# Performance work log

Hardware: AMD Instinct MI355X
Metric: run time of the kernel (lower is better)

## Reference

```python
import jax, jax.numpy as jnp
import numpy as np

VOX = 0.1
XMIN, YMIN, ZMIN = -20.0, -20.0, -2.0
XMAX, YMAX, ZMAX = 20.0, 20.0, 3.0
GX, GY = 400, 400          # grid size from (40m / 0.1m)
P = 32                     # max_points_per_voxel
K = 60000                  # max_num_voxels
N = 2_000_000              # total points
B = 4                      # batch size
SUB = 120                  # points drawn from a 120x120 sub-grid so uniques (<=57600) <= K


def setup_inputs() -> dict:
    key = jax.random.key(0)
    kb, kx, ky, kz, ki, ku, kv = jax.random.split(key, 7)
    b = jax.random.randint(kb, (N,), 0, B).astype(jnp.float32)
    xi = jax.random.randint(kx, (N,), 0, SUB).astype(jnp.float32)
    yi = jax.random.randint(ky, (N,), 0, SUB).astype(jnp.float32)
    ux = jax.random.uniform(ku, (N,))
    uy = jax.random.uniform(kv, (N,))
    x = XMIN + (xi + ux * 0.999) * VOX
    y = YMIN + (yi + uy * 0.999) * VOX
    z = jax.random.uniform(kz, (N,), minval=ZMIN, maxval=ZMAX - 1e-3)
    r = jax.random.uniform(ki, (N,))
    points = jnp.stack([b, x, y, z, r], axis=1)  # [N,5]
    return {"points": points, "batch_size": B}


def reference(points, batch_size):
    # in-range mask (identity for our generated data, but kept for fidelity)
    mask = ((points[:, 1] >= XMIN) & (points[:, 1] < XMAX)
            & (points[:, 2] >= YMIN) & (points[:, 2] < YMAX)
            & (points[:, 3] >= ZMIN) & (points[:, 3] < ZMAX))
    bi = points[:, 0].astype(jnp.int32)
    xi = jnp.clip(((points[:, 1] - XMIN) / VOX).astype(jnp.int32), 0, GX - 1)
    yi = jnp.clip(((points[:, 2] - YMIN) / VOX).astype(jnp.int32), 0, GY - 1)
    # flat voxel id; numeric order == lexicographic (b,x,y) order as in torch.unique(dim=0)
    flat = bi * (GX * GY) + xi * GY + yi
    sentinel = jnp.int32(batch_size * GX * GY)
    flat = jnp.where(mask, flat, sentinel)
    uniq, inv = jnp.unique(flat, size=K, fill_value=sentinel, return_inverse=True)
    inv = inv.astype(jnp.int32)

    # points per voxel (clamped to slot capacity)
    counts = jax.ops.segment_sum(mask.astype(jnp.int32), inv, num_segments=K)
    counts = jnp.minimum(counts, P)

    # slot = rank of each point within its voxel, in original point order
    order = jnp.argsort(inv)                      # stable
    sinv = inv[order]
    first = jnp.searchsorted(sinv, sinv, side='left')
    ranks = (jnp.arange(N) - first).astype(jnp.int32)
    slot = jnp.zeros(N, jnp.int32).at[order].set(ranks)

    # scatter point features into fixed-size voxel slots; overflow/out-of-range dropped
    rows = jnp.where(mask, inv, K)                # K is OOB -> dropped
    voxels = jnp.zeros((K, P, 4), points.dtype).at[rows, slot].set(
        points[:, 1:5], mode='drop')

    # decode sorted unique flat ids back to (batch, x, y)
    cb = uniq // (GX * GY)
    rem = uniq % (GX * GY)
    coors = jnp.stack([cb, rem // GY, rem % GY], axis=1)
    return voxels, counts, coors
```

## Files before the change

### kernel.cpp

```cpp
#include <hip/hip_runtime.h>

namespace {

constexpr int GX = 400, GY = 400;
constexpr int P = 32;
constexpr int K = 60000;
constexpr int MCAP = 128;
constexpr int NB = 4;
constexpr int NVOX = NB * GX * GY;
constexpr int SCAN_CHUNK = 1024;
constexpr int NBLK = (NVOX + 1 + SCAN_CHUNK - 1) / SCAN_CHUNK;
constexpr int OCC_PAD = NBLK * SCAN_CHUNK;

constexpr unsigned A20 = 0x779B1u;
constexpr unsigned mulinv20(unsigned a) {
  unsigned x = a;
  for (int i = 0; i < 6; ++i) x *= 2u - a * x;
  return x & 0xFFFFFu;
}
constexpr unsigned AINV20 = mulinv20(A20);
static_assert(((A20 * AINV20) & 0xFFFFFu) == 1u, "bad inverse");

constexpr int NBUK3 = 512;
constexpr int JH = 2048;
constexpr int CAP3 = 5120;
constexpr int PPB = 4096;
constexpr int IPT = PPB / 256;

constexpr float XMINf = -20.f, YMINf = -20.f, ZMINf = -2.f;
constexpr float XMAXf =  20.f, YMAXf =  20.f, ZMAXf =  3.f;

constexpr int OUT_CNT = K * P * 4;
constexpr int OUT_COR = OUT_CNT + K;

typedef float floatx2 __attribute__((ext_vector_type(2)));

__device__ __forceinline__ int bin_of(float v) {
  return (int)((v + 20.0f) * 10.0f);
}

__device__ __forceinline__ bool point_voxel(const float* __restrict__ pt, int& flat) {
  float x = pt[1], y = pt[2], z = pt[3];
  bool m = (x >= XMINf) & (x < XMAXf) & (y >= YMINf) & (y < YMAXf)
         & (z >= ZMINf) & (z < ZMAXf);
  if (!m) return false;
  int bi = (int)pt[0];
  int xi = min(max(bin_of(x), 0), GX - 1);
  int yi = min(max(bin_of(y), 0), GY - 1);
  flat = bi * (GX * GY) + xi * GY + yi;
  return true;
}

__device__ __forceinline__ unsigned bf16rne(float f) {
  unsigned u = __float_as_uint(f);
  return ((u + 0x7fffu + ((u >> 16) & 1u)) >> 16) & 0xffffu;
}
__device__ __forceinline__ float bf16dq(unsigned h) {
  return __uint_as_float(h << 16);
}

__global__ void __launch_bounds__(256) k_mark_bucket(
    const float* __restrict__ pts, int n, int* __restrict__ occ,
    int* __restrict__ bcur, unsigned* __restrict__ akey,
    uint2* __restrict__ afeat) {
  __shared__ int hist[512], lb[512], gb[512], ofs[512];
  __shared__ unsigned st[PPB];
  __shared__ uint2 stf[PPB];
  __shared__ unsigned short stb[PPB];
  __shared__ int ps[256];
  __shared__ int tot_s;
  int t = threadIdx.x;
  for (int j = t; j < 512; j += 256) hist[j] = 0;
  __syncthreads();

  int base = blockIdx.x * PPB;
  int bk[IPT]; unsigned rec[IPT]; uint2 ft[IPT];
  #pragma unroll
  for (int j = 0; j < IPT; ++j) {
    int i = base + j * 256 + t;
    bk[j] = -1;
    if (i < n) {
      const float* pp = pts + (size_t)i * 5;
      int flat;
      if (point_voxel(pp, flat)) {
        occ[flat] = 1;
        unsigned u = ((unsigned)flat * A20) & 0xFFFFFu;
        bk[j] = (int)(u >> 11);
        rec[j] = ((u & 0x7FFu) << 21) | (unsigned)i;
        ft[j].x = bf16rne(pp[1]) | (bf16rne(pp[2]) << 16);
        ft[j].y = bf16rne(pp[3]) | (bf16rne(pp[4]) << 16);
      }
    }
    if (bk[j] >= 0) atomicAdd(&hist[bk[j]], 1);
  }
  __syncthreads();
  int h0 = hist[2 * t], h1 = hist[2 * t + 1];
  int local = h0 + h1;
  ps[t] = local;
  __syncthreads();
  for (int o = 1; o < 256; o <<= 1) {
    int add = (t >= o) ? ps[t - o] : 0;
    __syncthreads();
    ps[t] += add;
    __syncthreads();
  }
  int excl = ps[t] - local;
  lb[2 * t] = excl;          ofs[2 * t] = excl;
  lb[2 * t + 1] = excl + h0; ofs[2 * t + 1] = excl + h0;
  if (t == 255) tot_s = ps[255];
  __syncthreads();
  #pragma unroll
  for (int j = 0; j < IPT; ++j) {
    if (bk[j] >= 0) {
      int pos = atomicAdd(&ofs[bk[j]], 1);
      st[pos] = rec[j];
      stf[pos] = ft[j];
      stb[pos] = (unsigned short)bk[j];
    }
  }
  __syncthreads();
  for (int b = t; b < NBUK3; b += 256) {
    int nb = hist[b];
    gb[b] = nb ? atomicAdd(&bcur[b], nb) : 0;
  }
  __syncthreads();
  int tot = tot_s;
  for (int e = t; e < tot; e += 256) {
    int b = stb[e];
    int dst = gb[b] + (e - lb[b]);
    if (dst < CAP3) {
      size_t a = (size_t)b * CAP3 + dst;
      akey[a] = st[e];
      afeat[a] = stf[e];
    }
  }
}

__global__ void k_bsum(const int* __restrict__ occ, int* __restrict__ bsum) {
  __shared__ int wsums[4];
  int t = threadIdx.x, wid = t >> 6, lane = t & 63;
  int base = blockIdx.x * SCAN_CHUNK;
  int4 v = ((const int4*)(occ + base))[t];
  int s = v.x + v.y + v.z + v.w;
  for (int o = 32; o > 0; o >>= 1) s += __shfl_xor(s, o, 64);
  if (lane == 0) wsums[wid] = s;
  __syncthreads();
  if (t == 0) bsum[blockIdx.x] = wsums[0] + wsums[1] + wsums[2] + wsums[3];
}

__global__ void k_scanb(int* __restrict__ bsum) {
  __shared__ int lds[1024];
  int t = threadIdx.x;
  int v = (t < NBLK) ? bsum[t] : 0;
  lds[t] = v;
  __syncthreads();
  for (int o = 1; o < 1024; o <<= 1) {
    int add = (t >= o) ? lds[t - o] : 0;
    __syncthreads();
    lds[t] += add;
    __syncthreads();
  }
  if (t < NBLK) bsum[t] = lds[t] - v;
  if (t == NBLK - 1) bsum[NBLK] = lds[t];
}

__global__ void k_rank(int* __restrict__ occ, const int* __restrict__ bsum,
                       int* __restrict__ uniq) {
  __shared__ int wsums[4];
  int t = threadIdx.x, wid = t >> 6, lane = t & 63;
  int base = blockIdx.x * SCAN_CHUNK;
  int4 v = ((const int4*)(occ + base))[t];
  int tsum = v.x + v.y + v.z + v.w;
  int sc = tsum;
  for (int o = 1; o < 64; o <<= 1) {
    int u = __shfl_up(sc, o, 64);
    if (lane >= o) sc += u;
  }
  if (lane == 63) wsums[wid] = sc;
  __syncthreads();
  int woff = 0;
  for (int w = 0; w < wid; ++w) woff += wsums[w];
  int p = bsum[blockIdx.x] + woff + (sc - tsum);
  int e0 = base + t * 4;
  int4 r;
  r.x = p; if (v.x) { if (p < K) uniq[p] = e0 + 0; ++p; }
  r.y = p; if (v.y) { if (p < K) uniq[p] = e0 + 1; ++p; }
  r.z = p; if (v.z) { if (p < K) uniq[p] = e0 + 2; ++p; }
  r.w = p; if (v.w) { if (p < K) uniq[p] = e0 + 3; ++p; }
  ((int4*)(occ + base))[t] = r;
}

__global__ void __launch_bounds__(256) k_build2(
    unsigned* __restrict__ akey, unsigned short* __restrict__ gpos,
    const int* __restrict__ bcur, const int* __restrict__ rank,
    const int* __restrict__ nuq_p, int* __restrict__ voxoff,
    int* __restrict__ vcnt) {
  __shared__ unsigned st[CAP3];
  __shared__ int hist[JH], scn[JH], cur[JH];
  __shared__ int ps[256];
  int b = blockIdx.x, t = threadIdx.x;
  int tot = min(bcur[b], CAP3);
  for (int j = t; j < JH; j += 256) hist[j] = 0;
  __syncthreads();
  unsigned* keys = akey + (size_t)b * CAP3;
  for (int i = t; i < tot; i += 256) {
    unsigned kk = keys[i];
    st[i] = kk;
    atomicAdd(&hist[kk >> 21], 1);
  }
  __syncthreads();
  int h[8]; int local = 0;
  #pragma unroll
  for (int u = 0; u < 8; ++u) { h[u] = hist[8 * t + u]; local += h[u]; }
  ps[t] = local;
  __syncthreads();
  for (int o = 1; o < 256; o <<= 1) {
    int add = (t >= o) ? ps[t - o] : 0;
    __syncthreads();
    ps[t] += add;
    __syncthreads();
  }
  int run = ps[t] - local;
  #pragma unroll
  for (int u = 0; u < 8; ++u) { scn[8 * t + u] = run; cur[8 * t + u] = run; run += h[u]; }
  __syncthreads();
  int cbase = b * CAP3;
  for (int i = t; i < tot; i += 256) {
    unsigned kk = st[i];
    int slot = atomicAdd(&cur[kk >> 21], 1);
    keys[slot] = kk & 0x1FFFFFu;
    gpos[cbase + slot] = (unsigned short)i;
  }
  int nq = min(nuq_p[0], K);
  for (int j = t; j < JH; j += 256) {
    if (hist[j] > 0) {
      unsigned u = ((unsigned)b << 11) | (unsigned)j;
      int flat = (int)((u * AINV20) & 0xFFFFFu);
      int k = rank[flat];
      if (k >= 0 && k < nq) {
        voxoff[k] = cbase + scn[j];
        vcnt[k] = hist[j];
      }
    }
  }
}

__global__ void __launch_bounds__(256) k_final_g(
    const unsigned* __restrict__ akey, const unsigned short* __restrict__ gpos,
    const uint2* __restrict__ afeat, const int* __restrict__ uniq,
    const int* __restrict__ voxoff, const int* __restrict__ vcnt,
    const int* __restrict__ nuq_p, float* __restrict__ out) {
  int wid = threadIdx.x >> 6, lane = threadIdx.x & 63;
  int k = blockIdx.x * 4 + wid;
  if (k >= K) return;
  int nq = min(nuq_p[0], K);
  const unsigned UMAX = 0xffffffffu;
  int s = lane >> 1, hh = lane & 1;

  int c_tot = 0, c_out = 0, off = 0;
  if (k < nq) {
    off = voxoff[k];
    int c = vcnt[k];
    c_tot = min(c, MCAP);
    c_out = min(c, P);
  }

  unsigned pos_s = 0u;
  if (c_tot > 0) {
    if (c_tot <= 64) {
      unsigned key = (lane < c_tot) ? akey[off + lane] : UMAX;
      unsigned pos = (lane < c_tot) ? (unsigned)gpos[off + lane] : 0u;
      for (int kk = 2; kk <= 64; kk <<= 1) {
        for (int d = kk >> 1; d >= 1; d >>= 1) {
          unsigned pk = __shfl_xor(key, d, 64);
          unsigned pq = __shfl_xor(pos, d, 64);
          bool tmin = ((lane & d) == 0) == ((lane & kk) == 0);
          bool sw = tmin ? (pk < key) : (pk > key);
          if (sw) { key = pk; pos = pq; }
        }
      }
      pos_s = __shfl(pos, s, 64);
    } else {
      unsigned k0 = (lane < c_tot) ? akey[off + lane] : UMAX;
      unsigned p0 = (lane < c_tot) ? (unsigned)gpos[off + lane] : 0u;
      unsigned k1 = (lane + 64 < c_tot) ? akey[off + 64 + lane] : UMAX;
      unsigned p1 = (lane + 64 < c_tot) ? (unsigned)gpos[off + 64 + lane] : 0u;
      #pragma unroll
      for (int ph = 1; ph <= 7; ++ph) {
        int kk = 1 << ph;
        bool up = ((lane & (kk >> 1)) == 0);
        #pragma unroll
        for (int d = kk >> 1; d >= 2; d >>= 1) {
          int dl = d >> 1;
          unsigned q0 = __shfl_xor(k0, dl, 64), r0 = __shfl_xor(p0, dl, 64);
          unsigned q1 = __shfl_xor(k1, dl, 64), r1 = __shfl_xor(p1, dl, 64);
          bool low = ((lane & dl) == 0);
          if (low == up) {
            if (q0 < k0) { k0 = q0; p0 = r0; }
            if (q1 < k1) { k1 = q1; p1 = r1; }
          } else {
            if (q0 > k0) { k0 = q0; p0 = r0; }
            if (q1 > k1) { k1 = q1; p1 = r1; }
          }
        }
        bool sw = up ? (k1 < k0) : (k1 > k0);
        if (sw) {
          unsigned tk = k0; k0 = k1; k1 = tk;
          unsigned tp = p0; p0 = p1; p1 = tp;
        }
      }
      unsigned a0 = __shfl(p0, s >> 1, 64);
      unsigned a1 = __shfl(p1, s >> 1, 64);
      pos_s = (s & 1) ? a1 : a0;
    }
  }

  uint2 fv = make_uint2(0u, 0u);
  if (s < c_out) {
    int b = off / CAP3;
    fv = afeat[(size_t)b * CAP3 + pos_s];
  }
  float va, vb;
  if (hh == 0) { va = bf16dq(fv.x & 0xffffu); vb = bf16dq(fv.x >> 16); }
  else         { va = bf16dq(fv.y & 0xffffu); vb = bf16dq(fv.y >> 16); }
  floatx2 val = {va, vb};
  __builtin_nontemporal_store(val, (floatx2*)(out + (size_t)k * (P * 4)) + lane);

  if (lane == 0) {
    out[OUT_CNT + k] = (float)c_out;
    int f = (k < nq) ? uniq[k] : NVOX;
    int cb = f / (GX * GY), rem = f % (GX * GY);
    out[OUT_COR + (size_t)k * 3 + 0] = (float)cb;
    out[OUT_COR + (size_t)k * 3 + 1] = (float)(rem / GY);
    out[OUT_COR + (size_t)k * 3 + 2] = (float)(rem % GY);
  }
}

__global__ void k_mark(const float* __restrict__ pts, int n,
                       int* __restrict__ occ, int* __restrict__ pflat) {
  int i = blockIdx.x * blockDim.x + threadIdx.x;
  if (i >= n) return;
  int flat = -1;
  if (point_voxel(pts + (size_t)i * 5, flat)) occ[flat] = 1;
  if (pflat) pflat[i] = flat;
}

__global__ void k_append(const int* __restrict__ pflat, int n,
                         const int* __restrict__ rank, int* __restrict__ cnt,
                         unsigned* __restrict__ vox) {
  int i = blockIdx.x * blockDim.x + threadIdx.x;
  if (i >= n) return;
  int f = pflat[i];
  if (f < 0) return;
  int v = rank[f];
  if (v >= K) return;
  int pos = atomicAdd(&cnt[v], 1);
  if (pos < MCAP) vox[(size_t)v * MCAP + pos] = (unsigned)i;
}

__global__ void k_append_fb(const float* __restrict__ pts, int n,
                            const int* __restrict__ rank, int* __restrict__ cnt,
                            unsigned* __restrict__ vox) {
  int i = blockIdx.x * blockDim.x + threadIdx.x;
  if (i >= n) return;
  int flat;
  if (!point_voxel(pts + (size_t)i * 5, flat)) return;
  int v = rank[flat];
  if (v >= K) return;
  int pos = atomicAdd(&cnt[v], 1);
  if (pos < MCAP) vox[(size_t)v * MCAP + pos] = (unsigned)i;
}

__global__ void __launch_bounds__(256) k_final_d(
    const float* __restrict__ pts, const int* __restrict__ uniq,
    const int* __restrict__ cnt, const int* __restrict__ nuq_p,
    float* __restrict__ out) {
  int wid = threadIdx.x >> 6, lane = threadIdx.x & 63;
  int k = blockIdx.x * 4 + wid;
  if (k >= K) return;
  int nuq = min(nuq_p[0], K);
  int c_tot = 0, c_out = 0;
  if (k < nuq) {
    int c = cnt[k];
    c_tot = min(c, MCAP);
    c_out = min(c, P);
  }
  const unsigned UMAX = 0xffffffffu;
  const unsigned* row = (const unsigned*)out + (size_t)k * MCAP;
  uint2 q = ((const uint2*)row)[lane];
  unsigned v0 = (2 * lane     < c_tot) ? q.x : UMAX;
  unsigned v1 = (2 * lane + 1 < c_tot) ? q.y : UMAX;
  #pragma unroll
  for (int ph = 1; ph <= 7; ++ph) {
    int kk = 1 << ph;
    bool up = ((lane & (kk >> 1)) == 0);
    #pragma unroll
    for (int d = kk >> 1; d >= 2; d >>= 1) {
      int dl = d >> 1;
      unsigned p0 = __shfl_xor(v0, dl, 64);
      unsigned p1 = __shfl_xor(v1, dl, 64);
      bool low = ((lane & dl) == 0);
      if (low == up) { v0 = min(v0, p0); v1 = min(v1, p1); }
      else           { v0 = max(v0, p0); v1 = max(v1, p1); }
    }
    unsigned lo = min(v0, v1), hi = max(v0, v1);
    v0 = up ? lo : hi;
    v1 = up ? hi : lo;
  }
  int mys = lane >> 1, h = lane & 1;
  unsigned a0 = __shfl(v0, mys >> 1, 64);
  unsigned a1 = __shfl(v1, mys >> 1, 64);
  unsigned myidx = (mys & 1) ? a1 : a0;
  float a = 0.f, b = 0.f;
  if (mys < c_out) {
    const float* pp = pts + (size_t)myidx * 5;
    a = pp[1 + 2 * h];
    b = pp[2 + 2 * h];
  }
  float2* vout = (float2*)(out + (size_t)k * (P * 4));
  vout[lane] = make_float2(a, b);
  if (lane == 0) {
    out[OUT_CNT + k] = (float)c_out;
    int f = (k < nuq) ? uniq[k] : NVOX;
    int cb = f / (GX * GY), rem = f % (GX * GY);
    out[OUT_COR + (size_t)k * 3 + 0] = (float)cb;
    out[OUT_COR + (size_t)k * 3 + 1] = (float)(rem / GY);
    out[OUT_COR + (size_t)k * 3 + 2] = (float)(rem % GY);
  }
}

}

extern "C" void kernel_launch(void* const* d_in, const int* in_sizes, int n_in,
                              void* d_out, int out_size, void* d_ws, size_t ws_size,
                              hipStream_t stream) {
  const float* pts = (const float*)d_in[0];
  int n = in_sizes[0] / 5;
  float* out = (float*)d_out;
  int nb_pts = (n + 255) / 256;

  size_t o_occ   = 0;
  size_t o_bsum  = o_occ + OCC_PAD;
  size_t o_uniq  = o_bsum + NBLK + 1;
  size_t o_voff  = o_uniq + K;
  size_t o_vcnt  = o_voff + K;
  size_t o_bcur  = o_vcnt + K;
  size_t o_akey  = (o_bcur + NBUK3 + 3) & ~(size_t)3;
  size_t o_afeat = o_akey + (size_t)NBUK3 * CAP3;
  size_t o_gpos  = o_afeat + (size_t)NBUK3 * CAP3 * 2;
  size_t totA    = o_gpos + ((size_t)NBUK3 * CAP3 + 1) / 2;

  if (ws_size >= totA * sizeof(int) && n <= (1 << 21)) {
    int* occ   = (int*)d_ws + o_occ;
    int* bsum  = (int*)d_ws + o_bsum;
    int* uniq  = (int*)d_ws + o_uniq;
    int* voff  = (int*)d_ws + o_voff;
    int* vcnt  = (int*)d_ws + o_vcnt;
    int* bcur  = (int*)d_ws + o_bcur;
    unsigned* akey = (unsigned*)((int*)d_ws + o_akey);
    uint2* afeat   = (uint2*)((int*)d_ws + o_afeat);
    unsigned short* gpos = (unsigned short*)((int*)d_ws + o_gpos);
    const int* nuq_p = bsum + NBLK;

    hipMemsetAsync(occ, 0, (size_t)OCC_PAD * sizeof(int), stream);
    hipMemsetAsync(bcur, 0, (size_t)NBUK3 * sizeof(int), stream);
    k_mark_bucket<<<(n + PPB - 1) / PPB, 256, 0, stream>>>(pts, n, occ, bcur, akey, afeat);
    k_bsum  <<<NBLK, 256, 0, stream>>>(occ, bsum);
    k_scanb <<<1, 1024, 0, stream>>>(bsum);
    k_rank  <<<NBLK, 256, 0, stream>>>(occ, bsum, uniq);
    k_build2<<<NBUK3, 256, 0, stream>>>(akey, gpos, bcur, occ, nuq_p, voff, vcnt);
    k_final_g<<<(K + 3) / 4, 256, 0, stream>>>(akey, gpos, afeat, uniq, voff, vcnt, nuq_p, out);
  } else {
    int* occ  = (int*)d_ws;
    int* bsum = occ + OCC_PAD;
    int* uniq = bsum + (NBLK + 1);
    int* cnt  = uniq + K;
    size_t base_ints = (size_t)OCC_PAD + (NBLK + 1) + K + K;
    base_ints = (base_ints + 3) & ~(size_t)3;
    int* pflat = (int*)d_ws + base_ints;
    bool use_pflat = ws_size >= (base_ints + (size_t)n) * sizeof(int);

    hipMemsetAsync(occ, 0, (size_t)OCC_PAD * sizeof(int), stream);
    hipMemsetAsync(cnt, 0, (size_t)K * sizeof(int), stream);
    k_mark  <<<nb_pts, 256, 0, stream>>>(pts, n, occ, use_pflat ? pflat : nullptr);
    k_bsum  <<<NBLK, 256, 0, stream>>>(occ, bsum);
    k_scanb <<<1, 1024, 0, stream>>>(bsum);
    k_rank  <<<NBLK, 256, 0, stream>>>(occ, bsum, uniq);
    if (use_pflat)
      k_append<<<nb_pts, 256, 0, stream>>>(pflat, n, occ, cnt, (unsigned*)out);
    else
      k_append_fb<<<nb_pts, 256, 0, stream>>>(pts, n, occ, cnt, (unsigned*)out);
    k_final_d<<<(K + 3) / 4, 256, 0, stream>>>(pts, uniq, cnt, bsum + NBLK, out);
  }
}
```

Before: 127.9 us.

## Process voxels per bucket in final kernel and fill empty voxel slots separately

```diff
diff --git a/kernel.cpp b/kernel.cpp
--- a/kernel.cpp
+++ b/kernel.cpp
@@ -24,6 +24,7 @@
 constexpr int NBUK3 = 512;
 constexpr int JH = 2048;
 constexpr int CAP3 = 5120;
+constexpr int VCAP = 256;
 constexpr int PPB = 4096;
 constexpr int IPT = PPB / 256;
 
@@ -194,13 +195,16 @@
     unsigned* __restrict__ akey, unsigned short* __restrict__ gpos,
     const int* __restrict__ bcur, const int* __restrict__ rank,
     const int* __restrict__ nuq_p, int* __restrict__ voxoff,
-    int* __restrict__ vcnt) {
+    int* __restrict__ vcnt, unsigned* __restrict__ vtab,
+    int* __restrict__ bvcnt) {
   __shared__ unsigned st[CAP3];
   __shared__ int hist[JH], scn[JH], cur[JH];
   __shared__ int ps[256];
+  __shared__ int nv;
   int b = blockIdx.x, t = threadIdx.x;
   int tot = min(bcur[b], CAP3);
   for (int j = t; j < JH; j += 256) hist[j] = 0;
+  if (t == 0) nv = 0;
   __syncthreads();
   unsigned* keys = akey + (size_t)b * CAP3;
   for (int i = t; i < tot; i += 256) {
@@ -240,33 +244,37 @@
       if (k >= 0 && k < nq) {
         voxoff[k] = cbase + scn[j];
         vcnt[k] = hist[j];
+        int p = atomicAdd(&nv, 1);
+        if (p < VCAP) vtab[b * VCAP + p] = ((unsigned)j << 17) | (unsigned)k;
       }
     }
   }
-}
-
-__global__ void __launch_bounds__(256) k_final_g(
+  __syncthreads();
+  if (t == 0) bvcnt[b] = min(nv, VCAP);
+}
+
+__global__ void __launch_bounds__(512) k_final_b(
     const unsigned* __restrict__ akey, const unsigned short* __restrict__ gpos,
-    const uint2* __restrict__ afeat, const int* __restrict__ uniq,
-    const int* __restrict__ voxoff, const int* __restrict__ vcnt,
-    const int* __restrict__ nuq_p, float* __restrict__ out) {
+    const uint2* __restrict__ afeat, const int* __restrict__ voxoff,
+    const int* __restrict__ vcnt, const unsigned* __restrict__ vtab,
+    const int* __restrict__ bvcnt, float* __restrict__ out) {
+  int b = blockIdx.x;
   int wid = threadIdx.x >> 6, lane = threadIdx.x & 63;
-  int k = blockIdx.x * 4 + wid;
-  if (k >= K) return;
-  int nq = min(nuq_p[0], K);
+  int nvb = bvcnt[b];
   const unsigned UMAX = 0xffffffffu;
   int s = lane >> 1, hh = lane & 1;
-
-  int c_tot = 0, c_out = 0, off = 0;
-  if (k < nq) {
-    off = voxoff[k];
+  size_t fbase = (size_t)b * CAP3;
+
+  for (int v = wid; v < nvb; v += 8) {
+    unsigned ent = vtab[b * VCAP + v];
+    int j = (int)(ent >> 17);
+    int k = (int)(ent & 0x1FFFFu);
+    int off = voxoff[k];
     int c = vcnt[k];
-    c_tot = min(c, MCAP);
-    c_out = min(c, P);
-  }
-
-  unsigned pos_s = 0u;
-  if (c_tot > 0) {
+    int c_tot = min(c, MCAP);
+    int c_out = min(c, P);
+
+    unsigned pos_s = 0u;
     if (c_tot <= 64) {
       unsigned key = (lane < c_tot) ? akey[off + lane] : UMAX;
       unsigned pos = (lane < c_tot) ? (unsigned)gpos[off + lane] : 0u;
@@ -313,26 +321,41 @@
       unsigned a1 = __shfl(p1, s >> 1, 64);
       pos_s = (s & 1) ? a1 : a0;
     }
-  }
-
-  uint2 fv = make_uint2(0u, 0u);
-  if (s < c_out) {
-    int b = off / CAP3;
-    fv = afeat[(size_t)b * CAP3 + pos_s];
-  }
-  float va, vb;
-  if (hh == 0) { va = bf16dq(fv.x & 0xffffu); vb = bf16dq(fv.x >> 16); }
-  else         { va = bf16dq(fv.y & 0xffffu); vb = bf16dq(fv.y >> 16); }
-  floatx2 val = {va, vb};
-  __builtin_nontemporal_store(val, (floatx2*)(out + (size_t)k * (P * 4)) + lane);
-
+
+    uint2 fv = make_uint2(0u, 0u);
+    if (s < c_out) fv = afeat[fbase + pos_s];
+    float va, vb;
+    if (hh == 0) { va = bf16dq(fv.x & 0xffffu); vb = bf16dq(fv.x >> 16); }
+    else         { va = bf16dq(fv.y & 0xffffu); vb = bf16dq(fv.y >> 16); }
+    floatx2 val = {va, vb};
+    __builtin_nontemporal_store(val, (floatx2*)(out + (size_t)k * (P * 4)) + lane);
+
+    if (lane == 0) {
+      out[OUT_CNT + k] = (float)c_out;
+      unsigned u = ((unsigned)b << 11) | (unsigned)j;
+      int flat = (int)((u * AINV20) & 0xFFFFFu);
+      int cb = flat / (GX * GY), rem = flat % (GX * GY);
+      out[OUT_COR + (size_t)k * 3 + 0] = (float)cb;
+      out[OUT_COR + (size_t)k * 3 + 1] = (float)(rem / GY);
+      out[OUT_COR + (size_t)k * 3 + 2] = (float)(rem % GY);
+    }
+  }
+}
+
+__global__ void __launch_bounds__(256) k_fill(const int* __restrict__ nuq_p,
+                                              float* __restrict__ out) {
+  int wid = threadIdx.x >> 6, lane = threadIdx.x & 63;
+  int k = blockIdx.x * 4 + wid;
+  if (k >= K) return;
+  int nq = min(nuq_p[0], K);
+  if (k < nq) return;
+  floatx2 z = {0.f, 0.f};
+  __builtin_nontemporal_store(z, (floatx2*)(out + (size_t)k * (P * 4)) + lane);
   if (lane == 0) {
-    out[OUT_CNT + k] = (float)c_out;
-    int f = (k < nq) ? uniq[k] : NVOX;
-    int cb = f / (GX * GY), rem = f % (GX * GY);
-    out[OUT_COR + (size_t)k * 3 + 0] = (float)cb;
-    out[OUT_COR + (size_t)k * 3 + 1] = (float)(rem / GY);
-    out[OUT_COR + (size_t)k * 3 + 2] = (float)(rem % GY);
+    out[OUT_CNT + k] = 0.f;
+    out[OUT_COR + (size_t)k * 3 + 0] = (float)(NVOX / (GX * GY));
+    out[OUT_COR + (size_t)k * 3 + 1] = 0.f;
+    out[OUT_COR + (size_t)k * 3 + 2] = 0.f;
   }
 }
 
@@ -445,7 +468,9 @@
   size_t o_voff  = o_uniq + K;
   size_t o_vcnt  = o_voff + K;
   size_t o_bcur  = o_vcnt + K;
-  size_t o_akey  = (o_bcur + NBUK3 + 3) & ~(size_t)3;
+  size_t o_bvc   = o_bcur + NBUK3;
+  size_t o_vtab  = o_bvc + NBUK3;
+  size_t o_akey  = (o_vtab + (size_t)NBUK3 * VCAP + 3) & ~(size_t)3;
   size_t o_afeat = o_akey + (size_t)NBUK3 * CAP3;
   size_t o_gpos  = o_afeat + (size_t)NBUK3 * CAP3 * 2;
   size_t totA    = o_gpos + ((size_t)NBUK3 * CAP3 + 1) / 2;
@@ -457,6 +482,8 @@
     int* voff  = (int*)d_ws + o_voff;
     int* vcnt  = (int*)d_ws + o_vcnt;
     int* bcur  = (int*)d_ws + o_bcur;
+    int* bvcnt = (int*)d_ws + o_bvc;
+    unsigned* vtab = (unsigned*)((int*)d_ws + o_vtab);
     unsigned* akey = (unsigned*)((int*)d_ws + o_akey);
     uint2* afeat   = (uint2*)((int*)d_ws + o_afeat);
     unsigned short* gpos = (unsigned short*)((int*)d_ws + o_gpos);
@@ -468,8 +495,9 @@
     k_bsum  <<<NBLK, 256, 0, stream>>>(occ, bsum);
     k_scanb <<<1, 1024, 0, stream>>>(bsum);
     k_rank  <<<NBLK, 256, 0, stream>>>(occ, bsum, uniq);
-    k_build2<<<NBUK3, 256, 0, stream>>>(akey, gpos, bcur, occ, nuq_p, voff, vcnt);
-    k_final_g<<<(K + 3) / 4, 256, 0, stream>>>(akey, gpos, afeat, uniq, voff, vcnt, nuq_p, out);
+    k_build2<<<NBUK3, 256, 0, stream>>>(akey, gpos, bcur, occ, nuq_p, voff, vcnt, vtab, bvcnt);
+    k_final_b<<<NBUK3, 512, 0, stream>>>(akey, gpos, afeat, voff, vcnt, vtab, bvcnt, out);
+    k_fill  <<<(K + 3) / 4, 256, 0, stream>>>(nuq_p, out);
   } else {
     int* occ  = (int*)d_ws;
     int* bsum = occ + OCC_PAD;
```

Result: slower. 138.2 us (+8.0%).
